# Kernel tuning notes

Measured on AMD Instinct MI355X. Metric: run time of the kernel, lower is better.

The kernel has to match this reference:

```python
import jax, jax.numpy as jnp
import numpy as np
from jax import lax

B, CIN, COUT, H, W = 8, 256, 256, 96, 96


def _conv_bn(x, w, g, b, act):
    # 3x3 conv, stride 1, SAME padding (NCHW / OIHW), then per-channel affine (folded BN)
    y = lax.conv_general_dilated(x, w, (1, 1), 'SAME',
                                 dimension_numbers=('NCHW', 'OIHW', 'NCHW'))
    y = y * g[None, :, None, None] + b[None, :, None, None]
    return jax.nn.relu(y) if act else y


def setup_inputs() -> dict:
    key = jax.random.key(0)
    ks = jax.random.split(key, 16)
    def wgt(k, cout, cin):
        return jax.random.normal(k, (cout, cin, 3, 3), jnp.float32) * (1.0 / np.sqrt(cin * 9))
    def gb(k, c):
        k1, k2 = jax.random.split(k)
        return (1.0 + 0.1 * jax.random.normal(k1, (c,), jnp.float32),
                0.1 * jax.random.normal(k2, (c,), jnp.float32))
    g_p1, b_p1 = gb(ks[1], COUT); g_p2, b_p2 = gb(ks[3], COUT)
    g_p, b_p = gb(ks[5], COUT); g_c1, b_c1 = gb(ks[7], COUT); g_c2, b_c2 = gb(ks[9], COUT)
    return {
        'x': jax.random.normal(ks[0], (B, CIN, H, W), jnp.float32),
        'w_p1': wgt(ks[10], COUT, CIN), 'g_p1': g_p1, 'b_p1': b_p1,
        'w_p2': wgt(ks[11], COUT, CIN), 'g_p2': g_p2, 'b_p2': b_p2,
        'w_p': wgt(ks[12], COUT, COUT), 'g_p': g_p, 'b_p': b_p,
        'w_c1': wgt(ks[13], COUT, CIN), 'g_c1': g_c1, 'b_c1': b_c1,
        'w_c2': wgt(ks[14], COUT, COUT), 'g_c2': g_c2, 'b_c2': b_c2,
    }


def reference(x, w_p1, g_p1, b_p1, w_p2, g_p2, b_p2, w_p, g_p, b_p,
              w_c1, g_c1, b_c1, w_c2, g_c2, b_c2):
    # branch 1: conv -> TopPool (cummax up, i.e. reverse along H) -> BottomPool (cummax down)
    p1 = _conv_bn(x, w_p1, g_p1, b_p1, act=True)
    pool1 = lax.cummax(p1, axis=2, reverse=True)   # TopPool
    pool1 = lax.cummax(pool1, axis=2)              # BottomPool
    # branch 2: conv -> LeftPool (reverse along W) -> RightPool
    p2 = _conv_bn(x, w_p2, g_p2, b_p2, act=True)
    pool2 = lax.cummax(p2, axis=3, reverse=True)   # LeftPool
    pool2 = lax.cummax(pool2, axis=3)              # RightPool
    p_conv = _conv_bn(pool1 + pool2, w_p, g_p, b_p, act=False)
    conv1 = _conv_bn(x, w_c1, g_c1, b_c1, act=False)
    relu = jax.nn.relu(p_conv + conv1)
    return _conv_bn(relu, w_c2, g_c2, b_c2, act=True)
```

## Files before the change

kernel.cpp:

```cpp
#include <hip/hip_runtime.h>


typedef _Float16 f16x8 __attribute__((ext_vector_type(8)));
typedef _Float16 f16x4v __attribute__((ext_vector_type(4)));
typedef float f32x4 __attribute__((ext_vector_type(4)));

#define HP 98
#define WP 98
#define KTOT 2304
#define WSET (256*KTOT)
#define XPAD_E ((size_t)8*HP*WP*256)
#define UVP_E  ((size_t)8*98*256)
#define UV2_E  ((size_t)3*8*96*256)
#define WUV_SET 196608

__device__ __forceinline__ int xcd_swz(int bid, int nwg)
{
  return (bid & 7) * (nwg >> 3) + (bid >> 3);
}

#define BUF_B 12288
#define SMEM_B 24576

struct Ctx {
  unsigned goff[3];
  unsigned lds_stage;
  unsigned aoff;
  int wl, quad, wv;
  int b, h0, w0;
};

template<int TR>
__device__ __forceinline__ Ctx make_ctx(int spatial)
{
  Ctx c;
  c.b = spatial / 72;
  const int tt = spatial - c.b * 72;
  if (TR == 0) { const int ht = tt / 6,  wt = tt - ht * 6;  c.h0 = ht * 8;  c.w0 = wt * 16; }
  else         { const int ht = tt / 12, wt = tt - ht * 12; c.h0 = ht * 16; c.w0 = wt * 8;  }
  const int tid = threadIdx.x, lane = tid & 63;
  c.wv = tid >> 6;
  c.quad = lane >> 4; c.wl = lane & 15;
  c.aoff = (unsigned)(c.wv * 4 * 512 + c.wl * 32 + c.quad * 8);
  const unsigned base_hw = (unsigned)(c.b * HP + c.h0) * WP + c.w0;
#pragma unroll
  for (int t = 0; t < 3; ++t) {
    int pos = (c.wv * 3 + t) * 16 + (lane >> 2);
    if (pos > 179) pos = 179;
    const int wh = (TR == 0) ? pos / 18 : pos / 10;
    const int ww = (TR == 0) ? pos - wh * 18 : pos - wh * 10;
    c.goff[t] = (base_hw + (unsigned)(wh * WP + ww)) * 256u + (lane & 3) * 8u;
  }
  c.lds_stage = (unsigned)(c.wv * 3) * 1024u + (unsigned)lane * 16u;
  return c;
}

__device__ __forceinline__ void stage_cb(const _Float16* __restrict__ src,
                                         char* sbuf, const Ctx& c, int buf, int cb)
{
  char* l0 = sbuf + buf * BUF_B + c.lds_stage;
#pragma unroll
  for (int t = 0; t < 3; ++t) {
    const _Float16* g = src + c.goff[t] + cb * 32;
    __builtin_amdgcn_global_load_lds(
        (const __attribute__((address_space(1))) void*)g,
        (__attribute__((address_space(3))) void*)(l0 + t * 1024), 16, 0, 0);
  }
}

template<int TR>
__device__ __forceinline__ void conv_accum(const _Float16* __restrict__ src,
                                           const _Float16* __restrict__ wkb,
                                           char* sbuf, const Ctx& c, f32x4 acc[4][8])
{
  const _Float16* A0 = wkb + c.aoff;
  stage_cb(src, sbuf, c, 0, 0);
#pragma unroll 1
  for (int cb = 0; cb < 8; ++cb) {
    __syncthreads();
    if (cb < 7) stage_cb(src, sbuf, c, (cb + 1) & 1, cb + 1);
    const _Float16* B = (const _Float16*)(sbuf + (cb & 1) * BUF_B);
    const _Float16* A = A0 + cb * (9 * 8192);
#pragma unroll
    for (int o = 0; o < 3; ++o) {
      f16x8 cache[10];
#pragma unroll
      for (int r = 0; r < 10; ++r)
        cache[r] = (TR == 0)
            ? *(const f16x8*)(B + (r * 18 + c.wl + o) * 32 + c.quad * 8)
            : *(const f16x8*)(B + ((c.wl + o) * 10 + r) * 32 + c.quad * 8);
#pragma unroll
      for (int p = 0; p < 3; ++p) {
        const int tap = (TR == 0) ? p * 3 + o : o * 3 + p;
        f16x8 af[4];
#pragma unroll
        for (int i = 0; i < 4; ++i)
          af[i] = *(const f16x8*)(A + tap * 8192 + i * 512);
#pragma unroll
        for (int i = 0; i < 4; ++i)
#pragma unroll
          for (int j = 0; j < 8; ++j)
            acc[i][j] = __builtin_amdgcn_mfma_f32_16x16x32_f16(af[i], cache[j + p], acc[i][j], 0, 0, 0);
      }
    }
  }
  __syncthreads();
}

#define ZERO_ACC8(acc) \
  _Pragma("unroll") for (int i = 0; i < 4; ++i) \
  _Pragma("unroll") for (int j = 0; j < 8; ++j) acc[i][j] = (f32x4){0.f,0.f,0.f,0.f};

#define BUF_W 7168
#define SMEM_W 14336

struct Ctx4 {
  unsigned goff[2];
  unsigned lds_stage;
  unsigned aoff;
  int nrow;
  int wl, quad, wv;
  int b, h0, w0;
};

template<int TR>
__device__ __forceinline__ Ctx4 make_ctx4(int spatial)
{
  Ctx4 c;
  c.b = spatial / 144;
  const int tt = spatial - c.b * 144;
  if (TR == 0) { const int ht = tt / 6,  wt = tt - ht * 6;  c.h0 = ht * 4;  c.w0 = wt * 16; }
  else         { const int ht = tt / 24, wt = tt - ht * 24; c.h0 = ht * 16; c.w0 = wt * 4;  }
  const int tid = threadIdx.x, lane = tid & 63;
  c.wv = tid >> 6;
  c.quad = lane >> 4; c.wl = lane & 15;
  c.aoff = (unsigned)(c.wv * 4 * 512 + c.wl * 32 + c.quad * 8);
  const unsigned base_hw = (unsigned)(c.b * HP + c.h0) * WP + c.w0;
  const int r0 = c.wv * 2;
  c.nrow = (c.wv < 3) ? 2 : 1;
#pragma unroll
  for (int t = 0; t < 2; ++t) {
    int row = r0 + t; if (row > 6) row = 6;
    int pos = row * 16 + (lane >> 2);
    if (pos > 107) pos = 107;
    const int wh = (TR == 0) ? pos / 18 : pos / 6;
    const int ww = (TR == 0) ? pos - wh * 18 : pos - wh * 6;
    c.goff[t] = (base_hw + (unsigned)(wh * WP + ww)) * 256u + (lane & 3) * 8u;
  }
  c.lds_stage = (unsigned)r0 * 1024u + (unsigned)lane * 16u;
  return c;
}

__device__ __forceinline__ void stage_cb4(const _Float16* __restrict__ src,
                                          char* sbuf, const Ctx4& c, int buf, int cb)
{
  char* l0 = sbuf + buf * BUF_W + c.lds_stage;
#pragma unroll
  for (int t = 0; t < 2; ++t) {
    if (t < c.nrow) {
      const _Float16* g = src + c.goff[t] + cb * 32;
      __builtin_amdgcn_global_load_lds(
          (const __attribute__((address_space(1))) void*)g,
          (__attribute__((address_space(3))) void*)(l0 + t * 1024), 16, 0, 0);
    }
  }
}

template<int TR>
__device__ __forceinline__ void conv_accum4(const _Float16* __restrict__ src,
                                            const _Float16* __restrict__ wkb,
                                            char* sbuf, const Ctx4& c, f32x4 acc[4][4])
{
  const _Float16* A0 = wkb + c.aoff;
  stage_cb4(src, sbuf, c, 0, 0);
#pragma unroll 1
  for (int cb = 0; cb < 8; ++cb) {
    __syncthreads();
    if (cb < 7) stage_cb4(src, sbuf, c, (cb + 1) & 1, cb + 1);
    const _Float16* B = (const _Float16*)(sbuf + (cb & 1) * BUF_W);
    const _Float16* A = A0 + cb * (9 * 8192);
#pragma unroll
    for (int o = 0; o < 3; ++o) {
      f16x8 cache[6];
#pragma unroll
      for (int r = 0; r < 6; ++r)
        cache[r] = (TR == 0)
            ? *(const f16x8*)(B + (r * 18 + c.wl + o) * 32 + c.quad * 8)
            : *(const f16x8*)(B + ((c.wl + o) * 6 + r) * 32 + c.quad * 8);
#pragma unroll
      for (int p = 0; p < 3; ++p) {
        const int tap = (TR == 0) ? p * 3 + o : o * 3 + p;
        f16x8 af[4];
#pragma unroll
        for (int i = 0; i < 4; ++i)
          af[i] = *(const f16x8*)(A + tap * 8192 + i * 512);
#pragma unroll
        for (int i = 0; i < 4; ++i)
#pragma unroll
          for (int j = 0; j < 4; ++j)
            acc[i][j] = __builtin_amdgcn_mfma_f32_16x16x32_f16(af[i], cache[j + p], acc[i][j], 0, 0, 0);
      }
    }
  }
  __syncthreads();
}

__global__ __launch_bounds__(256, 2) void k_conv_p12(
    const _Float16* __restrict__ xpad, const _Float16* __restrict__ wk,
    const float* __restrict__ bias1, const float* __restrict__ bias2,
    float* __restrict__ u_pad, float* __restrict__ v_pad)
{
  __shared__ __align__(16) char smem[SMEM_B];
  const int lin = xcd_swz(blockIdx.x, 1152);
  const int set = lin >= 576;
  const int spatial = lin - set * 576;
  f32x4 acc[4][8];
  ZERO_ACC8(acc)
  if (set == 0) {
    Ctx c = make_ctx<0>(spatial);
    conv_accum<0>(xpad, wk, smem, c, acc);
#pragma unroll
    for (int i = 0; i < 4; ++i) {
      const int co = c.wv * 64 + i * 16 + c.quad * 4;
      const float4 bs = *(const float4*)(bias1 + co);
      float m0 = 0.f, m1 = 0.f, m2 = 0.f, m3 = 0.f;
#pragma unroll
      for (int j = 0; j < 8; ++j) {
        m0 = fmaxf(m0, acc[i][j][0] + bs.x);
        m1 = fmaxf(m1, acc[i][j][1] + bs.y);
        m2 = fmaxf(m2, acc[i][j][2] + bs.z);
        m3 = fmaxf(m3, acc[i][j][3] + bs.w);
      }
      unsigned* tgt = (unsigned*)(u_pad + ((size_t)c.b * 98 + (c.w0 + c.wl + 1)) * 256 + co);
      atomicMax(tgt + 0, __float_as_uint(m0));
      atomicMax(tgt + 1, __float_as_uint(m1));
      atomicMax(tgt + 2, __float_as_uint(m2));
      atomicMax(tgt + 3, __float_as_uint(m3));
    }
  } else {
    Ctx c = make_ctx<1>(spatial);
    conv_accum<1>(xpad, wk + WSET, smem, c, acc);
#pragma unroll
    for (int i = 0; i < 4; ++i) {
      const int co = c.wv * 64 + i * 16 + c.quad * 4;
      const float4 bs = *(const float4*)(bias2 + co);
      float m0 = 0.f, m1 = 0.f, m2 = 0.f, m3 = 0.f;
#pragma unroll
      for (int j = 0; j < 8; ++j) {
        m0 = fmaxf(m0, acc[i][j][0] + bs.x);
        m1 = fmaxf(m1, acc[i][j][1] + bs.y);
        m2 = fmaxf(m2, acc[i][j][2] + bs.z);
        m3 = fmaxf(m3, acc[i][j][3] + bs.w);
      }
      unsigned* tgt = (unsigned*)(v_pad + ((size_t)c.b * 98 + (c.h0 + c.wl + 1)) * 256 + co);
      atomicMax(tgt + 0, __float_as_uint(m0));
      atomicMax(tgt + 1, __float_as_uint(m1));
      atomicMax(tgt + 2, __float_as_uint(m2));
      atomicMax(tgt + 3, __float_as_uint(m3));
    }
  }
}

__global__ __launch_bounds__(256, 2) void k_uv1d(
    const float* __restrict__ u_pad, const float* __restrict__ v_pad,
    const _Float16* __restrict__ wuv, float* __restrict__ u2, float* __restrict__ v2)
{
  const int id = blockIdx.x;
  const int b = id & 7, cs = (id >> 3) % 3, t = id / 24;
  const float* src = t ? v_pad : u_pad;
  float* dst = t ? v2 : u2;
  const _Float16* A0 = wuv + (size_t)(t * 3 + cs) * WUV_SET;
  const int lane = threadIdx.x & 63, wv = threadIdx.x >> 6;
  const int quad = lane >> 4, l16 = lane & 15;

  f32x4 acc[4][6];
#pragma unroll
  for (int i = 0; i < 4; ++i)
#pragma unroll
    for (int j = 0; j < 6; ++j) acc[i][j] = (f32x4){0.f, 0.f, 0.f, 0.f};

#pragma unroll 1
  for (int kb = 0; kb < 24; ++kb) {
    const int dw = kb >> 3, cb = kb & 7;
    f16x8 bf[6];
#pragma unroll
    for (int j = 0; j < 6; ++j) {
      const int pos = j * 16 + l16;
      const float* p = src + ((size_t)b * 98 + (pos + dw)) * 256 + cb * 32 + quad * 8;
      const float4 x0 = *(const float4*)p;
      const float4 x1 = *(const float4*)(p + 4);
      f16x8 v;
      v[0] = (_Float16)x0.x; v[1] = (_Float16)x0.y; v[2] = (_Float16)x0.z; v[3] = (_Float16)x0.w;
      v[4] = (_Float16)x1.x; v[5] = (_Float16)x1.y; v[6] = (_Float16)x1.z; v[7] = (_Float16)x1.w;
      bf[j] = v;
    }
    f16x8 af[4];
#pragma unroll
    for (int i = 0; i < 4; ++i)
      af[i] = *(const f16x8*)(A0 + (size_t)(kb * 16 + wv * 4 + i) * 512 + l16 * 32 + quad * 8);
#pragma unroll
    for (int i = 0; i < 4; ++i)
#pragma unroll
      for (int j = 0; j < 6; ++j)
        acc[i][j] = __builtin_amdgcn_mfma_f32_16x16x32_f16(af[i], bf[j], acc[i][j], 0, 0, 0);
  }
#pragma unroll
  for (int i = 0; i < 4; ++i)
#pragma unroll
    for (int j = 0; j < 6; ++j) {
      const int pos = j * 16 + l16;
      const int co = wv * 64 + i * 16 + quad * 4;
      *(f32x4*)(dst + ((size_t)(cs * 8 + b) * 96 + pos) * 256 + co) = acc[i][j];
    }
}

__global__ __launch_bounds__(256, 3) void k_conv_c1f(
    const _Float16* __restrict__ xpad, const _Float16* __restrict__ wkc1,
    const float* __restrict__ bias_p, const float* __restrict__ bias_c1,
    const float* __restrict__ u2, const float* __restrict__ v2,
    _Float16* __restrict__ rpad)
{
  __shared__ __align__(16) char smem[SMEM_W];
  const int lin = xcd_swz(blockIdx.x, 1152);
  Ctx4 c = make_ctx4<0>(lin);
  f32x4 acc[4][4];
#pragma unroll
  for (int i = 0; i < 4; ++i)
#pragma unroll
    for (int j = 0; j < 4; ++j) acc[i][j] = (f32x4){0.f, 0.f, 0.f, 0.f};
  conv_accum4<0>(xpad, wkc1, smem, c, acc);

  const int w = c.w0 + c.wl;
  const int wcase = (w == 0) ? 0 : ((w == 95) ? 2 : 1);
#pragma unroll
  for (int i = 0; i < 4; ++i) {
    const int co = c.wv * 64 + i * 16 + c.quad * 4;
    float4 bs = *(const float4*)(bias_p + co);
    const float4 b2 = *(const float4*)(bias_c1 + co);
    bs.x += b2.x; bs.y += b2.y; bs.z += b2.z; bs.w += b2.w;
#pragma unroll
    for (int j = 0; j < 4; ++j) {
      const int h = c.h0 + j;
      const int hcase = (h == 0) ? 0 : ((h == 95) ? 2 : 1);
      const float4 uq = *(const float4*)(u2 + ((size_t)(hcase * 8 + c.b) * 96 + w) * 256 + co);
      const float4 vq = *(const float4*)(v2 + ((size_t)(wcase * 8 + c.b) * 96 + h) * 256 + co);
      f16x4v pk;
      pk[0] = (_Float16)fmaxf(acc[i][j][0] + bs.x + uq.x + vq.x, 0.f);
      pk[1] = (_Float16)fmaxf(acc[i][j][1] + bs.y + uq.y + vq.y, 0.f);
      pk[2] = (_Float16)fmaxf(acc[i][j][2] + bs.z + uq.z + vq.z, 0.f);
      pk[3] = (_Float16)fmaxf(acc[i][j][3] + bs.w + uq.w + vq.w, 0.f);
      *(f16x4v*)(rpad + ((size_t)(c.b * HP + h + 1) * WP + w + 1) * 256 + co) = pk;
    }
  }
}

__global__ __launch_bounds__(256, 3) void k_conv_c2(
    const _Float16* __restrict__ rpad, const _Float16* __restrict__ wkc2,
    const float* __restrict__ bias, float* __restrict__ dout)
{
  __shared__ __align__(16) char smem[SMEM_W];
  const int lin = xcd_swz(blockIdx.x, 1152);
  Ctx4 c = make_ctx4<0>(lin);
  f32x4 acc[4][4];
#pragma unroll
  for (int i = 0; i < 4; ++i)
#pragma unroll
    for (int j = 0; j < 4; ++j) acc[i][j] = (f32x4){0.f, 0.f, 0.f, 0.f};
  conv_accum4<0>(rpad, wkc2, smem, c, acc);

  const int w = c.w0 + c.wl;
#pragma unroll
  for (int j = 0; j < 4; ++j) {
    const int h = c.h0 + j;
    float* op = dout + (size_t)c.b * 2359296 + h * 96 + w;
#pragma unroll
    for (int i = 0; i < 4; ++i) {
      const int co = c.wv * 64 + i * 16 + c.quad * 4;
      const float4 bs = *(const float4*)(bias + co);
      op[(size_t)(co + 0) * 9216] = fmaxf(acc[i][j][0] + bs.x, 0.f);
      op[(size_t)(co + 1) * 9216] = fmaxf(acc[i][j][1] + bs.y, 0.f);
      op[(size_t)(co + 2) * 9216] = fmaxf(acc[i][j][2] + bs.z, 0.f);
      op[(size_t)(co + 3) * 9216] = fmaxf(acc[i][j][3] + bs.w, 0.f);
    }
  }
}

__global__ void k_border(_Float16* __restrict__ xpad, _Float16* __restrict__ rpad)
{
  const int idx = blockIdx.x, b = blockIdx.y;
  _Float16* buf = blockIdx.z ? rpad : xpad;
  int h, w;
  if (idx < 98)       { h = 0;  w = idx; }
  else if (idx < 196) { h = 97; w = idx - 98; }
  else { const int r = idx - 196; h = 1 + (r >> 1); w = (r & 1) ? 97 : 0; }
  buf[((size_t)(b * HP + h) * WP + w) * 256 + threadIdx.x] = (_Float16)0.f;
}

__global__ void k_pack_x(const float* __restrict__ x, _Float16* __restrict__ xpad)
{
  __shared__ float tile[32][33];
  const int bh = blockIdx.x;
  const int b = bh / 96, h = bh - b * 96;
  const int c0 = blockIdx.y * 32, w0 = blockIdx.z * 32;
  const int tx = threadIdx.x & 31, ty = threadIdx.x >> 5;
#pragma unroll
  for (int i = 0; i < 4; ++i) {
    int cI = c0 + ty + i * 8;
    tile[ty + i * 8][tx] = x[(((size_t)b * 256 + cI) * 96 + h) * 96 + w0 + tx];
  }
  __syncthreads();
#pragma unroll
  for (int i = 0; i < 4; ++i) {
    int w = w0 + ty + i * 8;
    xpad[((size_t)(b * HP + h + 1) * WP + (w + 1)) * 256 + c0 + tx] =
        (_Float16)tile[tx][ty + i * 8];
  }
}

__global__ void k_repack_w(const float* w0, const float* g0, const float* w1, const float* g1,
                           const float* w2, const float* g2, const float* w3, const float* g3,
                           const float* w4, const float* g4, _Float16* __restrict__ wk)
{
  const int set = blockIdx.y;
  const float* w; const float* g;
  switch (set) {
    case 0: w = w0; g = g0; break;
    case 1: w = w1; g = g1; break;
    case 2: w = w2; g = g2; break;
    case 3: w = w3; g = g3; break;
    default: w = w4; g = g4; break;
  }
  const int t = blockIdx.x * 256 + threadIdx.x;
  const int co = t >> 8, ci = t & 255;
  const int cb = ci >> 5, kk = ci & 31, cog = co >> 4, m = co & 15;
  const float gv = g[co];
  const float* src = w + ((size_t)co * 256 + ci) * 9;
  _Float16* dst = wk + (size_t)set * WSET + cog * 512 + m * 32 + kk;
#pragma unroll
  for (int tap = 0; tap < 9; ++tap)
    dst[(cb * 9 + tap) * 8192] = (_Float16)(src[tap] * gv);
}

__global__ void k_repack_uvw(const float* __restrict__ wp, const float* __restrict__ gp,
                             _Float16* __restrict__ wuv)
{
  const int tcs = blockIdx.y;
  const int tt = tcs / 3, cs = tcs - tt * 3;
  const int idx = blockIdx.x * 256 + threadIdx.x;
  const int co = idx >> 8, ci = idx & 255;
  const float gv = gp[co];
  const float* src = wp + ((size_t)co * 256 + ci) * 9;
  const int lo = (cs == 0) ? 1 : 0, hi = (cs == 2) ? 1 : 2;
  _Float16* base = wuv + (size_t)tcs * WUV_SET;
#pragma unroll
  for (int d = 0; d < 3; ++d) {
    float s = 0.f;
    for (int e = lo; e <= hi; ++e)
      s += (tt == 0) ? src[e * 3 + d] : src[d * 3 + e];
    const int k = d * 256 + ci;
    const int kb = k >> 5, kk = k & 31;
    base[(size_t)(kb * 16 + (co >> 4)) * 512 + (co & 15) * 32 + kk] = (_Float16)(s * gv);
  }
}

extern "C" void kernel_launch(void* const* d_in, const int* in_sizes, int n_in,
                              void* d_out, int out_size, void* d_ws, size_t ws_size,
                              hipStream_t stream)
{
  const float* x    = (const float*)d_in[0];
  const float* w_p1 = (const float*)d_in[1];
  const float* g_p1 = (const float*)d_in[2];
  const float* b_p1 = (const float*)d_in[3];
  const float* w_p2 = (const float*)d_in[4];
  const float* g_p2 = (const float*)d_in[5];
  const float* b_p2 = (const float*)d_in[6];
  const float* w_p  = (const float*)d_in[7];
  const float* g_p  = (const float*)d_in[8];
  const float* b_p  = (const float*)d_in[9];
  const float* w_c1 = (const float*)d_in[10];
  const float* g_c1 = (const float*)d_in[11];
  const float* b_c1 = (const float*)d_in[12];
  const float* w_c2 = (const float*)d_in[13];
  const float* g_c2 = (const float*)d_in[14];
  const float* b_c2 = (const float*)d_in[15];

  char* ws = (char*)d_ws;
  size_t off = 0;
  _Float16* x_pad = (_Float16*)(ws + off); off += XPAD_E * 2;
  _Float16* r_pad = (_Float16*)(ws + off); off += XPAD_E * 2;
  _Float16* wks   = (_Float16*)(ws + off); off += (size_t)5 * WSET * 2;
  _Float16* wuv   = (_Float16*)(ws + off); off += (size_t)6 * WUV_SET * 2;
  float*    u_pad = (float*)(ws + off);    off += UVP_E * 4;
  float*    v_pad = (float*)(ws + off);    off += UVP_E * 4;
  float*    u2    = (float*)(ws + off);    off += UV2_E * 4;
  float*    v2    = (float*)(ws + off);    off += UV2_E * 4;
  (void)ws_size; (void)in_sizes; (void)n_in; (void)out_size;

  hipMemsetAsync(u_pad, 0, UVP_E * 4, stream);
  hipMemsetAsync(v_pad, 0, UVP_E * 4, stream);

  k_border    <<<dim3(388, 8, 2), 256, 0, stream>>>(x_pad, r_pad);
  k_pack_x    <<<dim3(768, 8, 3), 256, 0, stream>>>(x, x_pad);
  k_repack_w  <<<dim3(256, 5),    256, 0, stream>>>(w_p1, g_p1, w_p2, g_p2, w_p, g_p,
                                                    w_c1, g_c1, w_c2, g_c2, wks);
  k_repack_uvw<<<dim3(256, 6),    256, 0, stream>>>(w_p, g_p, wuv);
  k_conv_p12  <<<1152, 256, 0, stream>>>(x_pad, wks, b_p1, b_p2, u_pad, v_pad);
  k_uv1d      <<<48,   256, 0, stream>>>(u_pad, v_pad, wuv, u2, v2);
  k_conv_c1f  <<<1152, 256, 0, stream>>>(x_pad, wks + (size_t)3 * WSET, b_p, b_c1,
                                         u2, v2, r_pad);
  k_conv_c2   <<<1152, 256, 0, stream>>>(r_pad, wks + (size_t)4 * WSET, b_c2,
                                         (float*)d_out);
}
```

Before: 602.5 us.

## Split conv blocks into two 128-thread halves over output channels

All three conv kernels now run 128-thread blocks (2 waves), and each block covers half the 256 output channels (selected by ch) over a full 8x16 spatial tile. The p12 grid doubles to 2304, while c1f and c2 move from the 4x16 tile to the 8x16 tile at the same block count. The aim is more MFMA work per staged input tile and less LDS footprint per unit of work. In exchange, each input tile is loaded twice (once per channel half), and each wave now issues six staging loads per channel block.

```diff
diff --git a/kernel.cpp b/kernel.cpp
--- a/kernel.cpp
+++ b/kernel.cpp
@@ -22,8 +22,8 @@
 #define BUF_B 12288
 #define SMEM_B 24576
 
-struct Ctx {
-  unsigned goff[3];
+struct CtxH {
+  unsigned goff[6];
   unsigned lds_stage;
   unsigned aoff;
   int wl, quad, wv;
@@ -31,9 +31,9 @@
 };
 
 template<int TR>
-__device__ __forceinline__ Ctx make_ctx(int spatial)
-{
-  Ctx c;
+__device__ __forceinline__ CtxH make_ctxH(int spatial, int ch)
+{
+  CtxH c;
   c.b = spatial / 72;
   const int tt = spatial - c.b * 72;
   if (TR == 0) { const int ht = tt / 6,  wt = tt - ht * 6;  c.h0 = ht * 8;  c.w0 = wt * 16; }
@@ -41,26 +41,26 @@
   const int tid = threadIdx.x, lane = tid & 63;
   c.wv = tid >> 6;
   c.quad = lane >> 4; c.wl = lane & 15;
-  c.aoff = (unsigned)(c.wv * 4 * 512 + c.wl * 32 + c.quad * 8);
+  c.aoff = (unsigned)((ch * 8 + c.wv * 4) * 512 + c.wl * 32 + c.quad * 8);
   const unsigned base_hw = (unsigned)(c.b * HP + c.h0) * WP + c.w0;
 #pragma unroll
-  for (int t = 0; t < 3; ++t) {
-    int pos = (c.wv * 3 + t) * 16 + (lane >> 2);
+  for (int t = 0; t < 6; ++t) {
+    int pos = (c.wv * 6 + t) * 16 + (lane >> 2);
     if (pos > 179) pos = 179;
     const int wh = (TR == 0) ? pos / 18 : pos / 10;
     const int ww = (TR == 0) ? pos - wh * 18 : pos - wh * 10;
     c.goff[t] = (base_hw + (unsigned)(wh * WP + ww)) * 256u + (lane & 3) * 8u;
   }
-  c.lds_stage = (unsigned)(c.wv * 3) * 1024u + (unsigned)lane * 16u;
+  c.lds_stage = (unsigned)(c.wv * 6) * 1024u + (unsigned)lane * 16u;
   return c;
 }
 
-__device__ __forceinline__ void stage_cb(const _Float16* __restrict__ src,
-                                         char* sbuf, const Ctx& c, int buf, int cb)
+__device__ __forceinline__ void stage_cbH(const _Float16* __restrict__ src,
+                                          char* sbuf, const CtxH& c, int buf, int cb)
 {
   char* l0 = sbuf + buf * BUF_B + c.lds_stage;
 #pragma unroll
-  for (int t = 0; t < 3; ++t) {
+  for (int t = 0; t < 6; ++t) {
     const _Float16* g = src + c.goff[t] + cb * 32;
     __builtin_amdgcn_global_load_lds(
         (const __attribute__((address_space(1))) void*)g,
@@ -69,16 +69,16 @@
 }
 
 template<int TR>
-__device__ __forceinline__ void conv_accum(const _Float16* __restrict__ src,
-                                           const _Float16* __restrict__ wkb,
-                                           char* sbuf, const Ctx& c, f32x4 acc[4][8])
+__device__ __forceinline__ void conv_accumH(const _Float16* __restrict__ src,
+                                            const _Float16* __restrict__ wkb,
+                                            char* sbuf, const CtxH& c, f32x4 acc[4][8])
 {
   const _Float16* A0 = wkb + c.aoff;
-  stage_cb(src, sbuf, c, 0, 0);
+  stage_cbH(src, sbuf, c, 0, 0);
 #pragma unroll 1
   for (int cb = 0; cb < 8; ++cb) {
     __syncthreads();
-    if (cb < 7) stage_cb(src, sbuf, c, (cb + 1) & 1, cb + 1);
+    if (cb < 7) stage_cbH(src, sbuf, c, (cb + 1) & 1, cb + 1);
     const _Float16* B = (const _Float16*)(sbuf + (cb & 1) * BUF_B);
     const _Float16* A = A0 + cb * (9 * 8192);
 #pragma unroll
@@ -111,117 +111,24 @@
   _Pragma("unroll") for (int i = 0; i < 4; ++i) \
   _Pragma("unroll") for (int j = 0; j < 8; ++j) acc[i][j] = (f32x4){0.f,0.f,0.f,0.f};
 
-#define BUF_W 7168
-#define SMEM_W 14336
-
-struct Ctx4 {
-  unsigned goff[2];
-  unsigned lds_stage;
-  unsigned aoff;
-  int nrow;
-  int wl, quad, wv;
-  int b, h0, w0;
-};
-
-template<int TR>
-__device__ __forceinline__ Ctx4 make_ctx4(int spatial)
-{
-  Ctx4 c;
-  c.b = spatial / 144;
-  const int tt = spatial - c.b * 144;
-  if (TR == 0) { const int ht = tt / 6,  wt = tt - ht * 6;  c.h0 = ht * 4;  c.w0 = wt * 16; }
-  else         { const int ht = tt / 24, wt = tt - ht * 24; c.h0 = ht * 16; c.w0 = wt * 4;  }
-  const int tid = threadIdx.x, lane = tid & 63;
-  c.wv = tid >> 6;
-  c.quad = lane >> 4; c.wl = lane & 15;
-  c.aoff = (unsigned)(c.wv * 4 * 512 + c.wl * 32 + c.quad * 8);
-  const unsigned base_hw = (unsigned)(c.b * HP + c.h0) * WP + c.w0;
-  const int r0 = c.wv * 2;
-  c.nrow = (c.wv < 3) ? 2 : 1;
-#pragma unroll
-  for (int t = 0; t < 2; ++t) {
-    int row = r0 + t; if (row > 6) row = 6;
-    int pos = row * 16 + (lane >> 2);
-    if (pos > 107) pos = 107;
-    const int wh = (TR == 0) ? pos / 18 : pos / 6;
-    const int ww = (TR == 0) ? pos - wh * 18 : pos - wh * 6;
-    c.goff[t] = (base_hw + (unsigned)(wh * WP + ww)) * 256u + (lane & 3) * 8u;
-  }
-  c.lds_stage = (unsigned)r0 * 1024u + (unsigned)lane * 16u;
-  return c;
-}
-
-__device__ __forceinline__ void stage_cb4(const _Float16* __restrict__ src,
-                                          char* sbuf, const Ctx4& c, int buf, int cb)
-{
-  char* l0 = sbuf + buf * BUF_W + c.lds_stage;
-#pragma unroll
-  for (int t = 0; t < 2; ++t) {
-    if (t < c.nrow) {
-      const _Float16* g = src + c.goff[t] + cb * 32;
-      __builtin_amdgcn_global_load_lds(
-          (const __attribute__((address_space(1))) void*)g,
-          (__attribute__((address_space(3))) void*)(l0 + t * 1024), 16, 0, 0);
-    }
-  }
-}
-
-template<int TR>
-__device__ __forceinline__ void conv_accum4(const _Float16* __restrict__ src,
-                                            const _Float16* __restrict__ wkb,
-                                            char* sbuf, const Ctx4& c, f32x4 acc[4][4])
-{
-  const _Float16* A0 = wkb + c.aoff;
-  stage_cb4(src, sbuf, c, 0, 0);
-#pragma unroll 1
-  for (int cb = 0; cb < 8; ++cb) {
-    __syncthreads();
-    if (cb < 7) stage_cb4(src, sbuf, c, (cb + 1) & 1, cb + 1);
-    const _Float16* B = (const _Float16*)(sbuf + (cb & 1) * BUF_W);
-    const _Float16* A = A0 + cb * (9 * 8192);
-#pragma unroll
-    for (int o = 0; o < 3; ++o) {
-      f16x8 cache[6];
-#pragma unroll
-      for (int r = 0; r < 6; ++r)
-        cache[r] = (TR == 0)
-            ? *(const f16x8*)(B + (r * 18 + c.wl + o) * 32 + c.quad * 8)
-            : *(const f16x8*)(B + ((c.wl + o) * 6 + r) * 32 + c.quad * 8);
-#pragma unroll
-      for (int p = 0; p < 3; ++p) {
-        const int tap = (TR == 0) ? p * 3 + o : o * 3 + p;
-        f16x8 af[4];
-#pragma unroll
-        for (int i = 0; i < 4; ++i)
-          af[i] = *(const f16x8*)(A + tap * 8192 + i * 512);
-#pragma unroll
-        for (int i = 0; i < 4; ++i)
-#pragma unroll
-          for (int j = 0; j < 4; ++j)
-            acc[i][j] = __builtin_amdgcn_mfma_f32_16x16x32_f16(af[i], cache[j + p], acc[i][j], 0, 0, 0);
-      }
-    }
-  }
-  __syncthreads();
-}
-
-__global__ __launch_bounds__(256, 2) void k_conv_p12(
+__global__ __launch_bounds__(128, 2) void k_conv_p12(
     const _Float16* __restrict__ xpad, const _Float16* __restrict__ wk,
     const float* __restrict__ bias1, const float* __restrict__ bias2,
     float* __restrict__ u_pad, float* __restrict__ v_pad)
 {
   __shared__ __align__(16) char smem[SMEM_B];
-  const int lin = xcd_swz(blockIdx.x, 1152);
-  const int set = lin >= 576;
-  const int spatial = lin - set * 576;
+  const int lin = xcd_swz(blockIdx.x, 2304);
+  const int set = lin >= 1152;
+  const int rem = lin - set * 1152;
+  const int spatial = rem >> 1, ch = rem & 1;
   f32x4 acc[4][8];
   ZERO_ACC8(acc)
   if (set == 0) {
-    Ctx c = make_ctx<0>(spatial);
-    conv_accum<0>(xpad, wk, smem, c, acc);
+    CtxH c = make_ctxH<0>(spatial, ch);
+    conv_accumH<0>(xpad, wk, smem, c, acc);
 #pragma unroll
     for (int i = 0; i < 4; ++i) {
-      const int co = c.wv * 64 + i * 16 + c.quad * 4;
+      const int co = (ch * 8 + c.wv * 4 + i) * 16 + c.quad * 4;
       const float4 bs = *(const float4*)(bias1 + co);
       float m0 = 0.f, m1 = 0.f, m2 = 0.f, m3 = 0.f;
 #pragma unroll
@@ -238,11 +145,11 @@
       atomicMax(tgt + 3, __float_as_uint(m3));
     }
   } else {
-    Ctx c = make_ctx<1>(spatial);
-    conv_accum<1>(xpad, wk + WSET, smem, c, acc);
+    CtxH c = make_ctxH<1>(spatial, ch);
+    conv_accumH<1>(xpad, wk + WSET, smem, c, acc);
 #pragma unroll
     for (int i = 0; i < 4; ++i) {
-      const int co = c.wv * 64 + i * 16 + c.quad * 4;
+      const int co = (ch * 8 + c.wv * 4 + i) * 16 + c.quad * 4;
       const float4 bs = *(const float4*)(bias2 + co);
       float m0 = 0.f, m1 = 0.f, m2 = 0.f, m3 = 0.f;
 #pragma unroll
@@ -314,32 +221,30 @@
     }
 }
 
-__global__ __launch_bounds__(256, 3) void k_conv_c1f(
+__global__ __launch_bounds__(128, 2) void k_conv_c1f(
     const _Float16* __restrict__ xpad, const _Float16* __restrict__ wkc1,
     const float* __restrict__ bias_p, const float* __restrict__ bias_c1,
     const float* __restrict__ u2, const float* __restrict__ v2,
     _Float16* __restrict__ rpad)
 {
-  __shared__ __align__(16) char smem[SMEM_W];
+  __shared__ __align__(16) char smem[SMEM_B];
   const int lin = xcd_swz(blockIdx.x, 1152);
-  Ctx4 c = make_ctx4<0>(lin);
-  f32x4 acc[4][4];
-#pragma unroll
-  for (int i = 0; i < 4; ++i)
-#pragma unroll
-    for (int j = 0; j < 4; ++j) acc[i][j] = (f32x4){0.f, 0.f, 0.f, 0.f};
-  conv_accum4<0>(xpad, wkc1, smem, c, acc);
+  const int spatial = lin >> 1, ch = lin & 1;
+  CtxH c = make_ctxH<0>(spatial, ch);
+  f32x4 acc[4][8];
+  ZERO_ACC8(acc)
+  conv_accumH<0>(xpad, wkc1, smem, c, acc);
 
   const int w = c.w0 + c.wl;
   const int wcase = (w == 0) ? 0 : ((w == 95) ? 2 : 1);
 #pragma unroll
   for (int i = 0; i < 4; ++i) {
-    const int co = c.wv * 64 + i * 16 + c.quad * 4;
+    const int co = (ch * 8 + c.wv * 4 + i) * 16 + c.quad * 4;
     float4 bs = *(const float4*)(bias_p + co);
     const float4 b2 = *(const float4*)(bias_c1 + co);
     bs.x += b2.x; bs.y += b2.y; bs.z += b2.z; bs.w += b2.w;
 #pragma unroll
-    for (int j = 0; j < 4; ++j) {
+    for (int j = 0; j < 8; ++j) {
       const int h = c.h0 + j;
       const int hcase = (h == 0) ? 0 : ((h == 95) ? 2 : 1);
       const float4 uq = *(const float4*)(u2 + ((size_t)(hcase * 8 + c.b) * 96 + w) * 256 + co);
@@ -354,28 +259,26 @@
   }
 }
 
-__global__ __launch_bounds__(256, 3) void k_conv_c2(
+__global__ __launch_bounds__(128, 2) void k_conv_c2(
     const _Float16* __restrict__ rpad, const _Float16* __restrict__ wkc2,
     const float* __restrict__ bias, float* __restrict__ dout)
 {
-  __shared__ __align__(16) char smem[SMEM_W];
+  __shared__ __align__(16) char smem[SMEM_B];
   const int lin = xcd_swz(blockIdx.x, 1152);
-  Ctx4 c = make_ctx4<0>(lin);
-  f32x4 acc[4][4];
-#pragma unroll
-  for (int i = 0; i < 4; ++i)
-#pragma unroll
-    for (int j = 0; j < 4; ++j) acc[i][j] = (f32x4){0.f, 0.f, 0.f, 0.f};
-  conv_accum4<0>(rpad, wkc2, smem, c, acc);
+  const int spatial = lin >> 1, ch = lin & 1;
+  CtxH c = make_ctxH<0>(spatial, ch);
+  f32x4 acc[4][8];
+  ZERO_ACC8(acc)
+  conv_accumH<0>(rpad, wkc2, smem, c, acc);
 
   const int w = c.w0 + c.wl;
 #pragma unroll
-  for (int j = 0; j < 4; ++j) {
+  for (int j = 0; j < 8; ++j) {
     const int h = c.h0 + j;
     float* op = dout + (size_t)c.b * 2359296 + h * 96 + w;
 #pragma unroll
     for (int i = 0; i < 4; ++i) {
-      const int co = c.wv * 64 + i * 16 + c.quad * 4;
+      const int co = (ch * 8 + c.wv * 4 + i) * 16 + c.quad * 4;
       const float4 bs = *(const float4*)(bias + co);
       op[(size_t)(co + 0) * 9216] = fmaxf(acc[i][j][0] + bs.x, 0.f);
       op[(size_t)(co + 1) * 9216] = fmaxf(acc[i][j][1] + bs.y, 0.f);
@@ -504,10 +407,10 @@
   k_repack_w  <<<dim3(256, 5),    256, 0, stream>>>(w_p1, g_p1, w_p2, g_p2, w_p, g_p,
                                                     w_c1, g_c1, w_c2, g_c2, wks);
   k_repack_uvw<<<dim3(256, 6),    256, 0, stream>>>(w_p, g_p, wuv);
-  k_conv_p12  <<<1152, 256, 0, stream>>>(x_pad, wks, b_p1, b_p2, u_pad, v_pad);
+  k_conv_p12  <<<2304, 128, 0, stream>>>(x_pad, wks, b_p1, b_p2, u_pad, v_pad);
   k_uv1d      <<<48,   256, 0, stream>>>(u_pad, v_pad, wuv, u2, v2);
-  k_conv_c1f  <<<1152, 256, 0, stream>>>(x_pad, wks + (size_t)3 * WSET, b_p, b_c1,
+  k_conv_c1f  <<<1152, 128, 0, stream>>>(x_pad, wks + (size_t)3 * WSET, b_p, b_c1,
                                          u2, v2, r_pad);
-  k_conv_c2   <<<1152, 256, 0, stream>>>(r_pad, wks + (size_t)4 * WSET, b_c2,
+  k_conv_c2   <<<1152, 128, 0, stream>>>(r_pad, wks + (size_t)4 * WSET, b_c2,
                                          (float*)d_out);
 }
```

Result: slower. 632.6 us (+5.0%).

## Retile pool-branch convs to 16x16 spatial tiles split across channel halves

Applied to the files above, without the earlier changes.

The p1/p2 branch conv kernel changes from 8x16 (or 16x8) spatial tiles covering all 256 output channels to 16x16 tiles covering half the output channels (128) per block. Each wave now holds 2 channel groups by 16 positions of accumulators instead of 4x8. The transposed branch uses a swizzled staging layout, so both branches share one inner loop. This shrinks the per-block halo overhead and uses fewer max-reduction atomics per output. The cost is doubled LDS per block (48KB), which may limit occupancy, and each input tile is now loaded twice, once per channel half.

```diff
diff --git a/kernel.cpp b/kernel.cpp
--- a/kernel.cpp
+++ b/kernel.cpp
@@ -19,48 +19,48 @@
   return (bid & 7) * (nwg >> 3) + (bid >> 3);
 }
 
-#define BUF_B 12288
-#define SMEM_B 24576
-
-struct Ctx {
-  unsigned goff[3];
+#define BUF_Q 24576
+#define SMEM_Q 49152
+
+struct CtxQ {
+  unsigned goff[6];
   unsigned lds_stage;
   unsigned aoff;
   int wl, quad, wv;
   int b, h0, w0;
 };
 
-template<int TR>
-__device__ __forceinline__ Ctx make_ctx(int spatial)
-{
-  Ctx c;
-  c.b = spatial / 72;
-  const int tt = spatial - c.b * 72;
-  if (TR == 0) { const int ht = tt / 6,  wt = tt - ht * 6;  c.h0 = ht * 8;  c.w0 = wt * 16; }
-  else         { const int ht = tt / 12, wt = tt - ht * 12; c.h0 = ht * 16; c.w0 = wt * 8;  }
+template<int SW>
+__device__ __forceinline__ CtxQ make_ctxQ(int spatial, int ch)
+{
+  CtxQ c;
+  c.b = spatial / 36;
+  const int tt = spatial - c.b * 36;
+  const int ht = tt / 6, wt = tt - ht * 6;
+  c.h0 = ht * 16; c.w0 = wt * 16;
   const int tid = threadIdx.x, lane = tid & 63;
   c.wv = tid >> 6;
   c.quad = lane >> 4; c.wl = lane & 15;
-  c.aoff = (unsigned)(c.wv * 4 * 512 + c.wl * 32 + c.quad * 8);
+  c.aoff = (unsigned)((ch * 8 + c.wv * 2) * 512 + c.wl * 32 + c.quad * 8);
   const unsigned base_hw = (unsigned)(c.b * HP + c.h0) * WP + c.w0;
 #pragma unroll
-  for (int t = 0; t < 3; ++t) {
-    int pos = (c.wv * 3 + t) * 16 + (lane >> 2);
-    if (pos > 179) pos = 179;
-    const int wh = (TR == 0) ? pos / 18 : pos / 10;
-    const int ww = (TR == 0) ? pos - wh * 18 : pos - wh * 10;
+  for (int t = 0; t < 6; ++t) {
+    int s = (c.wv * 6 + t) * 16 + (lane >> 2);
+    if (s > 323) s = 323;
+    const int x = s / 18, y = s - x * 18;
+    const int wh = SW ? y : x, ww = SW ? x : y;
     c.goff[t] = (base_hw + (unsigned)(wh * WP + ww)) * 256u + (lane & 3) * 8u;
   }
-  c.lds_stage = (unsigned)(c.wv * 3) * 1024u + (unsigned)lane * 16u;
+  c.lds_stage = (unsigned)(c.wv * 6) * 1024u + (unsigned)lane * 16u;
   return c;
 }
 
-__device__ __forceinline__ void stage_cb(const _Float16* __restrict__ src,
-                                         char* sbuf, const Ctx& c, int buf, int cb)
-{
-  char* l0 = sbuf + buf * BUF_B + c.lds_stage;
-#pragma unroll
-  for (int t = 0; t < 3; ++t) {
+__device__ __forceinline__ void stage_cbQ(const _Float16* __restrict__ src,
+                                          char* sbuf, const CtxQ& c, int buf, int cb)
+{
+  char* l0 = sbuf + buf * BUF_Q + c.lds_stage;
+#pragma unroll
+  for (int t = 0; t < 6; ++t) {
     const _Float16* g = src + c.goff[t] + cb * 32;
     __builtin_amdgcn_global_load_lds(
         (const __attribute__((address_space(1))) void*)g,
@@ -69,47 +69,47 @@
 }
 
 template<int TR>
-__device__ __forceinline__ void conv_accum(const _Float16* __restrict__ src,
-                                           const _Float16* __restrict__ wkb,
-                                           char* sbuf, const Ctx& c, f32x4 acc[4][8])
+__device__ __forceinline__ void conv_accumQ(const _Float16* __restrict__ src,
+                                            const _Float16* __restrict__ wkb,
+                                            char* sbuf, const CtxQ& c, f32x4 acc[2][16])
 {
   const _Float16* A0 = wkb + c.aoff;
-  stage_cb(src, sbuf, c, 0, 0);
+  stage_cbQ(src, sbuf, c, 0, 0);
 #pragma unroll 1
   for (int cb = 0; cb < 8; ++cb) {
     __syncthreads();
-    if (cb < 7) stage_cb(src, sbuf, c, (cb + 1) & 1, cb + 1);
-    const _Float16* B = (const _Float16*)(sbuf + (cb & 1) * BUF_B);
+    if (cb < 7) stage_cbQ(src, sbuf, c, (cb + 1) & 1, cb + 1);
+    const _Float16* B = (const _Float16*)(sbuf + (cb & 1) * BUF_Q);
     const _Float16* A = A0 + cb * (9 * 8192);
 #pragma unroll
     for (int o = 0; o < 3; ++o) {
-      f16x8 cache[10];
-#pragma unroll
-      for (int r = 0; r < 10; ++r)
-        cache[r] = (TR == 0)
-            ? *(const f16x8*)(B + (r * 18 + c.wl + o) * 32 + c.quad * 8)
-            : *(const f16x8*)(B + ((c.wl + o) * 10 + r) * 32 + c.quad * 8);
+      f16x8 af[3][2];
 #pragma unroll
       for (int p = 0; p < 3; ++p) {
         const int tap = (TR == 0) ? p * 3 + o : o * 3 + p;
-        f16x8 af[4];
-#pragma unroll
-        for (int i = 0; i < 4; ++i)
-          af[i] = *(const f16x8*)(A + tap * 8192 + i * 512);
-#pragma unroll
-        for (int i = 0; i < 4; ++i)
-#pragma unroll
-          for (int j = 0; j < 8; ++j)
-            acc[i][j] = __builtin_amdgcn_mfma_f32_16x16x32_f16(af[i], cache[j + p], acc[i][j], 0, 0, 0);
+#pragma unroll
+        for (int i = 0; i < 2; ++i)
+          af[p][i] = *(const f16x8*)(A + tap * 8192 + i * 512);
       }
+#pragma unroll
+      for (int jh = 0; jh < 2; ++jh) {
+        f16x8 cache[10];
+#pragma unroll
+        for (int r = 0; r < 10; ++r)
+          cache[r] = *(const f16x8*)(B + ((jh * 8 + r) * 18 + c.wl + o) * 32 + c.quad * 8);
+#pragma unroll
+        for (int p = 0; p < 3; ++p)
+#pragma unroll
+          for (int i = 0; i < 2; ++i)
+#pragma unroll
+            for (int j = 0; j < 8; ++j)
+              acc[i][jh * 8 + j] = __builtin_amdgcn_mfma_f32_16x16x32_f16(
+                  af[p][i], cache[j + p], acc[i][jh * 8 + j], 0, 0, 0);
+      }
     }
   }
   __syncthreads();
 }
-
-#define ZERO_ACC8(acc) \
-  _Pragma("unroll") for (int i = 0; i < 4; ++i) \
-  _Pragma("unroll") for (int j = 0; j < 8; ++j) acc[i][j] = (f32x4){0.f,0.f,0.f,0.f};
 
 #define BUF_W 7168
 #define SMEM_W 14336
@@ -123,14 +123,12 @@
   int b, h0, w0;
 };
 
-template<int TR>
 __device__ __forceinline__ Ctx4 make_ctx4(int spatial)
 {
   Ctx4 c;
   c.b = spatial / 144;
   const int tt = spatial - c.b * 144;
-  if (TR == 0) { const int ht = tt / 6,  wt = tt - ht * 6;  c.h0 = ht * 4;  c.w0 = wt * 16; }
-  else         { const int ht = tt / 24, wt = tt - ht * 24; c.h0 = ht * 16; c.w0 = wt * 4;  }
+  const int ht = tt / 6,  wt = tt - ht * 6;  c.h0 = ht * 4;  c.w0 = wt * 16;
   const int tid = threadIdx.x, lane = tid & 63;
   c.wv = tid >> 6;
   c.quad = lane >> 4; c.wl = lane & 15;
@@ -143,8 +141,7 @@
     int row = r0 + t; if (row > 6) row = 6;
     int pos = row * 16 + (lane >> 2);
     if (pos > 107) pos = 107;
-    const int wh = (TR == 0) ? pos / 18 : pos / 6;
-    const int ww = (TR == 0) ? pos - wh * 18 : pos - wh * 6;
+    const int wh = pos / 18, ww = pos - wh * 18;
     c.goff[t] = (base_hw + (unsigned)(wh * WP + ww)) * 256u + (lane & 3) * 8u;
   }
   c.lds_stage = (unsigned)r0 * 1024u + (unsigned)lane * 16u;
@@ -166,7 +163,6 @@
   }
 }
 
-template<int TR>
 __device__ __forceinline__ void conv_accum4(const _Float16* __restrict__ src,
                                             const _Float16* __restrict__ wkb,
                                             char* sbuf, const Ctx4& c, f32x4 acc[4][4])
@@ -184,12 +180,10 @@
       f16x8 cache[6];
 #pragma unroll
       for (int r = 0; r < 6; ++r)
-        cache[r] = (TR == 0)
-            ? *(const f16x8*)(B + (r * 18 + c.wl + o) * 32 + c.quad * 8)
-            : *(const f16x8*)(B + ((c.wl + o) * 6 + r) * 32 + c.quad * 8);
+        cache[r] = *(const f16x8*)(B + (r * 18 + c.wl + o) * 32 + c.quad * 8);
 #pragma unroll
       for (int p = 0; p < 3; ++p) {
-        const int tap = (TR == 0) ? p * 3 + o : o * 3 + p;
+        const int tap = p * 3 + o;
         f16x8 af[4];
 #pragma unroll
         for (int i = 0; i < 4; ++i)
@@ -210,22 +204,26 @@
     const float* __restrict__ bias1, const float* __restrict__ bias2,
     float* __restrict__ u_pad, float* __restrict__ v_pad)
 {
-  __shared__ __align__(16) char smem[SMEM_B];
+  __shared__ __align__(16) char smem[SMEM_Q];
   const int lin = xcd_swz(blockIdx.x, 1152);
   const int set = lin >= 576;
-  const int spatial = lin - set * 576;
-  f32x4 acc[4][8];
-  ZERO_ACC8(acc)
+  const int rem = lin - set * 576;
+  const int spatial = rem >> 1, ch = rem & 1;
+  f32x4 acc[2][16];
+#pragma unroll
+  for (int i = 0; i < 2; ++i)
+#pragma unroll
+    for (int j = 0; j < 16; ++j) acc[i][j] = (f32x4){0.f, 0.f, 0.f, 0.f};
   if (set == 0) {
-    Ctx c = make_ctx<0>(spatial);
-    conv_accum<0>(xpad, wk, smem, c, acc);
-#pragma unroll
-    for (int i = 0; i < 4; ++i) {
-      const int co = c.wv * 64 + i * 16 + c.quad * 4;
+    CtxQ c = make_ctxQ<0>(spatial, ch);
+    conv_accumQ<0>(xpad, wk, smem, c, acc);
+#pragma unroll
+    for (int i = 0; i < 2; ++i) {
+      const int co = (ch * 8 + c.wv * 2 + i) * 16 + c.quad * 4;
       const float4 bs = *(const float4*)(bias1 + co);
       float m0 = 0.f, m1 = 0.f, m2 = 0.f, m3 = 0.f;
 #pragma unroll
-      for (int j = 0; j < 8; ++j) {
+      for (int j = 0; j < 16; ++j) {
         m0 = fmaxf(m0, acc[i][j][0] + bs.x);
         m1 = fmaxf(m1, acc[i][j][1] + bs.y);
         m2 = fmaxf(m2, acc[i][j][2] + bs.z);
@@ -238,15 +236,15 @@
       atomicMax(tgt + 3, __float_as_uint(m3));
     }
   } else {
-    Ctx c = make_ctx<1>(spatial);
-    conv_accum<1>(xpad, wk + WSET, smem, c, acc);
-#pragma unroll
-    for (int i = 0; i < 4; ++i) {
-      const int co = c.wv * 64 + i * 16 + c.quad * 4;
+    CtxQ c = make_ctxQ<1>(spatial, ch);
+    conv_accumQ<1>(xpad, wk + WSET, smem, c, acc);
+#pragma unroll
+    for (int i = 0; i < 2; ++i) {
+      const int co = (ch * 8 + c.wv * 2 + i) * 16 + c.quad * 4;
       const float4 bs = *(const float4*)(bias2 + co);
       float m0 = 0.f, m1 = 0.f, m2 = 0.f, m3 = 0.f;
 #pragma unroll
-      for (int j = 0; j < 8; ++j) {
+      for (int j = 0; j < 16; ++j) {
         m0 = fmaxf(m0, acc[i][j][0] + bs.x);
         m1 = fmaxf(m1, acc[i][j][1] + bs.y);
         m2 = fmaxf(m2, acc[i][j][2] + bs.z);
@@ -322,13 +320,13 @@
 {
   __shared__ __align__(16) char smem[SMEM_W];
   const int lin = xcd_swz(blockIdx.x, 1152);
-  Ctx4 c = make_ctx4<0>(lin);
+  Ctx4 c = make_ctx4(lin);
   f32x4 acc[4][4];
 #pragma unroll
   for (int i = 0; i < 4; ++i)
 #pragma unroll
     for (int j = 0; j < 4; ++j) acc[i][j] = (f32x4){0.f, 0.f, 0.f, 0.f};
-  conv_accum4<0>(xpad, wkc1, smem, c, acc);
+  conv_accum4(xpad, wkc1, smem, c, acc);
 
   const int w = c.w0 + c.wl;
   const int wcase = (w == 0) ? 0 : ((w == 95) ? 2 : 1);
@@ -360,13 +358,13 @@
 {
   __shared__ __align__(16) char smem[SMEM_W];
   const int lin = xcd_swz(blockIdx.x, 1152);
-  Ctx4 c = make_ctx4<0>(lin);
+  Ctx4 c = make_ctx4(lin);
   f32x4 acc[4][4];
 #pragma unroll
   for (int i = 0; i < 4; ++i)
 #pragma unroll
     for (int j = 0; j < 4; ++j) acc[i][j] = (f32x4){0.f, 0.f, 0.f, 0.f};
-  conv_accum4<0>(rpad, wkc2, smem, c, acc);
+  conv_accum4(rpad, wkc2, smem, c, acc);
 
   const int w = c.w0 + c.wl;
 #pragma unroll
```

New measurement: 560.6 us. 1.07x faster.
